# Performance work log

Measured on AMD Instinct MI355X. Metric: run time of the kernel, lower is better.

Reference implementation:

```python
import jax, jax.numpy as jnp
import numpy as np

N_NODES = 50000
N_EDGES = 500000
N_GRAPHS = 256
F_XD = 78


def _linear_init(key, fan_in, fan_out):
    s = 1.0 / np.sqrt(fan_in)
    kw, kb = jax.random.split(key)
    W = jax.random.uniform(kw, (fan_in, fan_out), jnp.float32, -s, s)
    b = jax.random.uniform(kb, (fan_out,), jnp.float32, -s, s)
    return W, b


def setup_inputs() -> dict:
    key = jax.random.key(0)
    ks = jax.random.split(key, 12)
    x = jax.random.normal(ks[0], (N_NODES, F_XD), jnp.float32)
    edge_index = jax.random.randint(ks[1], (2, N_EDGES), 0, N_NODES, jnp.int32)
    # sorted graph assignment; every graph non-empty
    batch = ((jnp.arange(N_NODES) * N_GRAPHS) // N_NODES).astype(jnp.int32)
    T = jax.random.normal(ks[2], (N_GRAPHS,), jnp.float32)
    P = jax.random.normal(ks[3], (N_GRAPHS,), jnp.float32)
    W1, b1 = _linear_init(ks[4], F_XD, F_XD)
    W2, b2 = _linear_init(ks[5], F_XD, 2 * F_XD)
    W3, b3 = _linear_init(ks[6], 2 * F_XD, 4 * F_XD)
    Wg1, bg1 = _linear_init(ks[7], 4 * F_XD, 1024)
    Wg2, bg2 = _linear_init(ks[8], 1024, 128)
    Wf1, bf1 = _linear_init(ks[9], 130, 1024)
    Wf2, bf2 = _linear_init(ks[10], 1024, 512)
    Wo, bo = _linear_init(ks[11], 512, 1)
    return dict(x=x, edge_index=edge_index, batch=batch, T=T, P=P,
                W1=W1, b1=b1, W2=W2, b2=b2, W3=W3, b3=b3,
                Wg1=Wg1, bg1=bg1, Wg2=Wg2, bg2=bg2,
                Wf1=Wf1, bf1=bf1, Wf2=Wf2, bf2=bf2, Wo=Wo, bo=bo)


def _gcn_conv(x, W, b, src, dst, norm, n_nodes):
    # PyG GCNConv: out = scatter_add(norm * (xW)[src] -> dst) + b
    h = x @ W
    msg = h[src] * norm[:, None]  # [E+N, F_out] gather, memory-bound
    return jax.ops.segment_sum(msg, dst, num_segments=n_nodes) + b


def reference(x, edge_index, batch, T, P,
              W1, b1, W2, b2, W3, b3,
              Wg1, bg1, Wg2, bg2, Wf1, bf1, Wf2, bf2, Wo, bo):
    n = x.shape[0]
    loops = jnp.arange(n, dtype=edge_index.dtype)
    src = jnp.concatenate([edge_index[0], loops])
    dst = jnp.concatenate([edge_index[1], loops])
    # symmetric normalization deg^-1/2 (A+I) deg^-1/2
    deg = jax.ops.segment_sum(jnp.ones_like(dst, dtype=x.dtype), dst, num_segments=n)
    dinv = jax.lax.rsqrt(deg)  # deg >= 1 due to self loops
    norm = dinv[src] * dinv[dst]

    h = jax.nn.relu(_gcn_conv(x, W1, b1, src, dst, norm, n))
    h = jax.nn.relu(_gcn_conv(h, W2, b2, src, dst, norm, n))
    h = jax.nn.relu(_gcn_conv(h, W3, b3, src, dst, norm, n))

    # global max pool per graph
    g = jax.ops.segment_max(h, batch, num_segments=N_GRAPHS)
    g = jax.nn.relu(g @ Wg1 + bg1)  # dropout = identity (eval)
    g = g @ Wg2 + bg2

    xc = jnp.concatenate([g, T[:, None], P[:, None]], axis=1)  # [G, 130]
    xc = jax.nn.relu(xc @ Wf1 + bf1)
    xc = jax.nn.relu(xc @ Wf2 + bf2)
    return xc @ Wo + bo
```

## Files before the change

kernel.cpp:

```cpp
#include <hip/hip_runtime.h>
#include <cstdint>
#include <cstddef>

static constexpr int NN = 50000;
static constexpr int NE = 500000;
static constexpr int NG = 256;

typedef short  frag8  __attribute__((ext_vector_type(8)));
typedef float  f32x4  __attribute__((ext_vector_type(4)));
typedef unsigned short us8 __attribute__((ext_vector_type(8)));

__device__ __forceinline__ unsigned short bf16_rne(float f) {
  unsigned u = __builtin_bit_cast(unsigned, f);
  u += 0x7fffu + ((u >> 16) & 1u);
  return (unsigned short)(u >> 16);
}
__device__ __forceinline__ float bf16_to_f(unsigned short h) {
  unsigned u = ((unsigned)h) << 16;
  return __builtin_bit_cast(float, u);
}

__global__ void k_count(const int* __restrict__ dst, int* __restrict__ cnt, int E) {
  int i = blockIdx.x * blockDim.x + threadIdx.x;
  if (i < E) atomicAdd(&cnt[dst[i]], 1);
}

__global__ void k_scan_partial(const int* __restrict__ cnt, int* __restrict__ partial,
                               float* __restrict__ dinv, int n) {
  __shared__ int sdata[1024];
  int tid = threadIdx.x;
  int i = blockIdx.x * 1024 + tid;
  int v = (i < n) ? cnt[i] : 0;
  if (i < n) dinv[i] = rsqrtf((float)(v + 1));
  sdata[tid] = v;
  __syncthreads();
  for (int s = 512; s > 0; s >>= 1) {
    if (tid < s) sdata[tid] += sdata[tid + s];
    __syncthreads();
  }
  if (tid == 0) partial[blockIdx.x] = sdata[0];
}

__global__ void k_scan_small(int* __restrict__ partial, int nb) {
  if (threadIdx.x == 0) {
    int run = 0;
    for (int b = 0; b < nb; ++b) { int v = partial[b]; partial[b] = run; run += v; }
  }
}

__global__ void k_scan_final(const int* __restrict__ cnt, const int* __restrict__ partial,
                             int* __restrict__ rowptr, int n) {
  __shared__ int buf[1024];
  int tid = threadIdx.x;
  int i = blockIdx.x * 1024 + tid;
  int v = (i < n) ? cnt[i] : 0;
  buf[tid] = v;
  __syncthreads();
  for (int off = 1; off < 1024; off <<= 1) {
    int t = (tid >= off) ? buf[tid - off] : 0;
    __syncthreads();
    buf[tid] += t;
    __syncthreads();
  }
  int excl = buf[tid] - v + partial[blockIdx.x];
  if (i < n) rowptr[i] = excl;
  if (i == n - 1) rowptr[n] = excl + v;
}

__global__ void k_fill(const int* __restrict__ src, const int* __restrict__ dst,
                       const int* __restrict__ rowptr, int* __restrict__ cur,
                       const float* __restrict__ dinv,
                       int* __restrict__ csr_src, float* __restrict__ csr_val, int E) {
  int i = blockIdx.x * blockDim.x + threadIdx.x;
  if (i < E) {
    int d = dst[i];
    int old = atomicAdd(&cur[d], -1);
    int pos = rowptr[d] + old - 1;
    int s = src[i];
    csr_src[pos] = s;
    csr_val[pos] = dinv[s];
  }
}

__global__ void k_padx(const float* __restrict__ x, float* __restrict__ x80) {
  int idx = blockIdx.x * blockDim.x + threadIdx.x;
  if (idx < NN * 80) {
    int row = idx / 80, c = idx - row * 80;
    x80[idx] = (c < 78) ? x[row * 78 + c] : 0.f;
  }
}

template<int CH, int CHP, int EPW>
__global__ void k_agg_dec8(const float* __restrict__ hin, const int* __restrict__ rowptr,
                           const int* __restrict__ csr_src, const float* __restrict__ csr_val,
                           const float* __restrict__ dinv,
                           unsigned short* __restrict__ Ah, unsigned short* __restrict__ Al, int n) {
  constexpr int Kp = CHP * 8;
  int wid = (blockIdx.x * blockDim.x + threadIdx.x) >> 6;
  int lane = threadIdx.x & 63;
  if (wid >= n) return;
  const float4* hin4 = (const float4*)hin;
  int eoff = lane / CH;
  int fl = lane - eoff * CH;
  float a[8];
#pragma unroll
  for (int j = 0; j < 8; ++j) a[j] = 0.f;
  int e0 = rowptr[wid], e1 = rowptr[wid + 1];
  if (eoff < EPW) {
    int e = e0 + eoff;
    for (; e + EPW < e1; e += 2 * EPW) {
      int   s0 = csr_src[e];        float w0 = csr_val[e];
      int   s1 = csr_src[e + EPW];  float w1 = csr_val[e + EPW];
      float4 u0 = hin4[(size_t)s0 * (CH * 2) + fl * 2];
      float4 u1 = hin4[(size_t)s0 * (CH * 2) + fl * 2 + 1];
      float4 v0 = hin4[(size_t)s1 * (CH * 2) + fl * 2];
      float4 v1 = hin4[(size_t)s1 * (CH * 2) + fl * 2 + 1];
      a[0] += w0 * u0.x + w1 * v0.x;  a[1] += w0 * u0.y + w1 * v0.y;
      a[2] += w0 * u0.z + w1 * v0.z;  a[3] += w0 * u0.w + w1 * v0.w;
      a[4] += w0 * u1.x + w1 * v1.x;  a[5] += w0 * u1.y + w1 * v1.y;
      a[6] += w0 * u1.z + w1 * v1.z;  a[7] += w0 * u1.w + w1 * v1.w;
    }
    if (e < e1) {
      int s0 = csr_src[e]; float w0 = csr_val[e];
      float4 u0 = hin4[(size_t)s0 * (CH * 2) + fl * 2];
      float4 u1 = hin4[(size_t)s0 * (CH * 2) + fl * 2 + 1];
      a[0] += w0 * u0.x; a[1] += w0 * u0.y; a[2] += w0 * u0.z; a[3] += w0 * u0.w;
      a[4] += w0 * u1.x; a[5] += w0 * u1.y; a[6] += w0 * u1.z; a[7] += w0 * u1.w;
    }
  }
  float r[8];
#pragma unroll
  for (int j = 0; j < 8; ++j) r[j] = a[j];
#pragma unroll
  for (int g = 1; g < EPW; ++g) {
#pragma unroll
    for (int j = 0; j < 8; ++j) r[j] += __shfl(a[j], lane + g * CH);
  }
  if (lane < CH) {
    float dv = dinv[wid];
    float4 s0 = hin4[(size_t)wid * (CH * 2) + lane * 2];
    float4 s1 = hin4[(size_t)wid * (CH * 2) + lane * 2 + 1];
    float v[8] = { dv * (r[0] + dv * s0.x), dv * (r[1] + dv * s0.y),
                   dv * (r[2] + dv * s0.z), dv * (r[3] + dv * s0.w),
                   dv * (r[4] + dv * s1.x), dv * (r[5] + dv * s1.y),
                   dv * (r[6] + dv * s1.z), dv * (r[7] + dv * s1.w) };
    us8 hi, lo;
#pragma unroll
    for (int j = 0; j < 8; ++j) {
      unsigned short h = bf16_rne(v[j]);
      hi[j] = h;
      lo[j] = bf16_rne(v[j] - bf16_to_f(h));
    }
    size_t base = (size_t)wid * Kp + lane * 8;
    *(us8*)(Ah + base) = hi;
    *(us8*)(Al + base) = lo;
  } else if (lane >= 60) {
    int c = CH + (lane - 60);
    if (c < CHP) {
      us8 z;
#pragma unroll
      for (int j = 0; j < 8; ++j) z[j] = 0;
      size_t base = (size_t)wid * Kp + (size_t)c * 8;
      *(us8*)(Ah + base) = z;
      *(us8*)(Al + base) = z;
    }
  }
}

template<int K, int N, int Kp, int Np>
__global__ void k_wdec(const float* __restrict__ W, unsigned short* __restrict__ Wh,
                       unsigned short* __restrict__ Wl) {
  int idx = blockIdx.x * blockDim.x + threadIdx.x;
  if (idx >= Np * Kp) return;
  int n = idx / Kp, k = idx - n * Kp;
  float v = (n < N && k < K) ? W[k * N + n] : 0.f;
  unsigned short h = bf16_rne(v);
  Wh[idx] = h;
  Wl[idx] = bf16_rne(v - bf16_to_f(h));
}

template<int Kp, int Np, int NB, bool POOL>
__global__ __launch_bounds__(256) void k_mm_mfma(const unsigned short* __restrict__ Ahp,
                                                 const unsigned short* __restrict__ Alp,
                                                 const unsigned short* __restrict__ Wh,
                                                 const unsigned short* __restrict__ Wl,
                                                 const float* __restrict__ bias,
                                                 float* __restrict__ C,
                                                 const int* __restrict__ batch,
                                                 unsigned int* __restrict__ poolU,
                                                 int N, int M) {
  constexpr int NCB = Np / NB;
  constexpr int NT = NB / 16;
  constexpr int KS = Kp / 32;
  constexpr int KC = Kp / 8;
  constexpr int PITCH = Kp + 8;
  __shared__ unsigned short wlds[2 * NB * PITCH];
  unsigned short* whi = wlds;
  unsigned short* wlo = wlds + NB * PITCH;
  int tid = threadIdx.x;
  int w = tid >> 6, l = tid & 63;
  int m = l & 15, kg = l >> 4;
  int nwg = gridDim.x;
  int orig = blockIdx.x;
  int qd = nwg >> 3, rm = nwg & 7;
  int xcd = orig & 7, seq = orig >> 3;
  int wgid = (xcd < rm ? xcd * (qd + 1) : rm * (qd + 1) + (xcd - rm) * qd) + seq;
  int bc = wgid % NCB;
  int br = wgid / NCB;
  int row0 = br * 128;
  for (int i = tid; i < 2 * NB * KC; i += 256) {
    int mtx = i / (NB * KC);
    int j = i - mtx * (NB * KC);
    int n = j / KC, qq = j - n * KC;
    const unsigned short* src = mtx ? Wl : Wh;
    unsigned short* dst = mtx ? wlo : whi;
    *(us8*)&dst[n * PITCH + qq * 8] = *(const us8*)&src[(size_t)(bc * NB + n) * Kp + qq * 8];
  }
  frag8 ah0[KS], al0[KS], ah1[KS], al1[KS];
  size_t arow0 = (size_t)(row0 + 32 * w + m) * Kp + kg * 8;
  size_t arow1 = arow0 + (size_t)16 * Kp;
#pragma unroll
  for (int kk = 0; kk < KS; ++kk) {
    ah0[kk] = *(const frag8*)(Ahp + arow0 + kk * 32);
    al0[kk] = *(const frag8*)(Alp + arow0 + kk * 32);
    ah1[kk] = *(const frag8*)(Ahp + arow1 + kk * 32);
    al1[kk] = *(const frag8*)(Alp + arow1 + kk * 32);
  }
  __syncthreads();

  f32x4 zero4 = {0.f, 0.f, 0.f, 0.f};
  f32x4 acc0[NT], acc1[NT];
#pragma unroll
  for (int t = 0; t < NT; ++t) { acc0[t] = zero4; acc1[t] = zero4; }

#pragma unroll
  for (int kk = 0; kk < KS; ++kk) {
#pragma unroll
    for (int t = 0; t < NT; ++t) {
      int n = t * 16 + m;
      int co = kk * 32 + kg * 8;
      frag8 bh = *(const frag8*)&whi[n * PITCH + co];
      frag8 bl = *(const frag8*)&wlo[n * PITCH + co];
      acc0[t] = __builtin_amdgcn_mfma_f32_16x16x32_bf16(ah0[kk], bh, acc0[t], 0, 0, 0);
      acc0[t] = __builtin_amdgcn_mfma_f32_16x16x32_bf16(ah0[kk], bl, acc0[t], 0, 0, 0);
      acc0[t] = __builtin_amdgcn_mfma_f32_16x16x32_bf16(al0[kk], bh, acc0[t], 0, 0, 0);
      acc1[t] = __builtin_amdgcn_mfma_f32_16x16x32_bf16(ah1[kk], bh, acc1[t], 0, 0, 0);
      acc1[t] = __builtin_amdgcn_mfma_f32_16x16x32_bf16(ah1[kk], bl, acc1[t], 0, 0, 0);
      acc1[t] = __builtin_amdgcn_mfma_f32_16x16x32_bf16(al1[kk], bh, acc1[t], 0, 0, 0);
    }
  }
  if (!POOL) {
#pragma unroll
    for (int t = 0; t < NT; ++t) {
      int col = bc * NB + t * 16 + m;
      float b = (col < N) ? bias[col] : 0.f;
#pragma unroll
      for (int r = 0; r < 4; ++r) {
        int row = row0 + 32 * w + kg * 4 + r;
        float v0 = fmaxf(acc0[t][r] + b, 0.f);
        float v1 = fmaxf(acc1[t][r] + b, 0.f);
        C[(size_t)row * Np + col] = (col < N) ? v0 : 0.f;
        C[(size_t)(row + 16) * Np + col] = (col < N) ? v1 : 0.f;
      }
    }
  } else {
    int gA = batch[row0];
    int rbase = row0 + 32 * w + kg * 4;
    int cls[8];
#pragma unroll
    for (int r = 0; r < 4; ++r) {
      int ra = rbase + r, rb = rbase + 16 + r;
      cls[r]     = (ra < M) ? ((batch[ra] == gA) ? 1 : 2) : 0;
      cls[4 + r] = (rb < M) ? ((batch[rb] == gA) ? 1 : 2) : 0;
    }
#pragma unroll
    for (int t = 0; t < NT; ++t) {
      int col = bc * NB + t * 16 + m;
      float b = (col < N) ? bias[col] : 0.f;
      float m0 = 0.f, m1 = 0.f;
#pragma unroll
      for (int r = 0; r < 4; ++r) {
        float v0 = fmaxf(acc0[t][r] + b, 0.f);
        float v1 = fmaxf(acc1[t][r] + b, 0.f);
        if (cls[r] == 1)     m0 = fmaxf(m0, v0); else if (cls[r] == 2)     m1 = fmaxf(m1, v0);
        if (cls[4 + r] == 1) m0 = fmaxf(m0, v1); else if (cls[4 + r] == 2) m1 = fmaxf(m1, v1);
      }
      m0 = fmaxf(m0, __shfl_xor(m0, 16)); m0 = fmaxf(m0, __shfl_xor(m0, 32));
      m1 = fmaxf(m1, __shfl_xor(m1, 16)); m1 = fmaxf(m1, __shfl_xor(m1, 32));
      if (l < 16 && col < N) {
        if (m0 > 0.f) atomicMax(&poolU[(size_t)gA * 320 + col], __float_as_uint(m0));
        if (m1 > 0.f) atomicMax(&poolU[(size_t)(gA + 1) * 320 + col], __float_as_uint(m1));
      }
    }
  }
}

template<int Kp, int Np, int NB, int KSPLIT, bool RELU, int OUTMODE, int SOUT>
__global__ __launch_bounds__(256) void k_hmm(const unsigned short* __restrict__ Ahp,
                                             const unsigned short* __restrict__ Alp,
                                             const unsigned short* __restrict__ Wh,
                                             const unsigned short* __restrict__ Wl,
                                             const float* __restrict__ bias,
                                             float* __restrict__ partOrC,
                                             unsigned short* __restrict__ OutH,
                                             unsigned short* __restrict__ OutL) {
  constexpr int NCB = Np / NB;
  constexpr int NT = NB / 16;
  constexpr int KS = Kp / 32 / KSPLIT;
  constexpr int PITCH = 40;
  __shared__ unsigned short wlds[2 * NB * PITCH];
  unsigned short* whi = wlds;
  unsigned short* wlo = wlds + NB * PITCH;
  int tid = threadIdx.x;
  int w = tid >> 6, l = tid & 63;
  int m = l & 15, kg = l >> 4;
  int bc = blockIdx.x % NCB;
  int kc = (blockIdx.x / NCB) % KSPLIT;
  int br = blockIdx.x / (NCB * KSPLIT);
  int row0 = br * 64;
  int kk0 = kc * KS;
  f32x4 zero4 = {0.f, 0.f, 0.f, 0.f};
  f32x4 acc[NT];
#pragma unroll
  for (int t = 0; t < NT; ++t) acc[t] = zero4;

  for (int kk = 0; kk < KS; ++kk) {
    int kabs = (kk0 + kk) * 32;
    for (int i = tid; i < NB * 8; i += 256) {
      int mtx = i / (NB * 4);
      int j = i - mtx * (NB * 4);
      int n = j >> 2, q = j & 3;
      const unsigned short* src = mtx ? Wl : Wh;
      unsigned short* dst = mtx ? wlo : whi;
      *(us8*)&dst[n * PITCH + ((q ^ (n >> 3)) & 3) * 8] =
          *(const us8*)&src[(size_t)(bc * NB + n) * Kp + kabs + q * 8];
    }
    __syncthreads();
    size_t abase = (size_t)(row0 + 16 * w + m) * Kp + kabs + kg * 8;
    frag8 ah = *(const frag8*)(Ahp + abase);
    frag8 al = *(const frag8*)(Alp + abase);
#pragma unroll
    for (int t = 0; t < NT; ++t) {
      int n = t * 16 + m;
      int sc = ((kg ^ (n >> 3)) & 3) * 8;
      frag8 bh = *(const frag8*)&whi[n * PITCH + sc];
      frag8 bl = *(const frag8*)&wlo[n * PITCH + sc];
      acc[t] = __builtin_amdgcn_mfma_f32_16x16x32_bf16(ah, bh, acc[t], 0, 0, 0);
      acc[t] = __builtin_amdgcn_mfma_f32_16x16x32_bf16(ah, bl, acc[t], 0, 0, 0);
      acc[t] = __builtin_amdgcn_mfma_f32_16x16x32_bf16(al, bh, acc[t], 0, 0, 0);
    }
    __syncthreads();
  }
#pragma unroll
  for (int t = 0; t < NT; ++t) {
    int col = bc * NB + t * 16 + m;
#pragma unroll
    for (int r = 0; r < 4; ++r) {
      int row = row0 + 16 * w + kg * 4 + r;
      float v = acc[t][r];
      if (KSPLIT > 1) {
        partOrC[((size_t)(kc * 256) + row) * Np + col] = v;
      } else {
        v += bias[col];
        if (RELU) v = fmaxf(v, 0.f);
        if (OUTMODE == 0) {
          partOrC[(size_t)row * SOUT + col] = v;
        } else {
          unsigned short h = bf16_rne(v);
          OutH[(size_t)row * SOUT + col] = h;
          OutL[(size_t)row * SOUT + col] = bf16_rne(v - bf16_to_f(h));
        }
      }
    }
  }
}

template<int Np, int KSPLIT, bool RELU, int OUTMODE, int SOUT>
__global__ void k_comb(const float* __restrict__ part, const float* __restrict__ bias,
                       float* __restrict__ Cf, unsigned short* __restrict__ OutH,
                       unsigned short* __restrict__ OutL) {
  int idx = blockIdx.x * 256 + threadIdx.x;
  int row = idx / Np, col = idx - row * Np;
  float s = bias[col];
#pragma unroll
  for (int kc = 0; kc < KSPLIT; ++kc) s += part[((size_t)(kc * 256) + row) * Np + col];
  if (RELU) s = fmaxf(s, 0.f);
  if (OUTMODE == 0) {
    Cf[(size_t)row * SOUT + col] = s;
  } else {
    unsigned short h = bf16_rne(s);
    OutH[(size_t)row * SOUT + col] = h;
    OutL[(size_t)row * SOUT + col] = bf16_rne(s - bf16_to_f(h));
  }
}

__global__ void k_pool_dec(const unsigned int* __restrict__ poolU,
                           unsigned short* __restrict__ g0H, unsigned short* __restrict__ g0L) {
  int idx = blockIdx.x * 256 + threadIdx.x;
  float v = __uint_as_float(poolU[idx]);
  unsigned short h = bf16_rne(v);
  g0H[idx] = h;
  g0L[idx] = bf16_rne(v - bf16_to_f(h));
}

__global__ void k_tp(const float* __restrict__ T, const float* __restrict__ P,
                     unsigned short* __restrict__ xcH, unsigned short* __restrict__ xcL) {
  int m = threadIdx.x;
  float t = T[m], p = P[m];
  unsigned short th = bf16_rne(t), ph = bf16_rne(p);
  xcH[(size_t)m * 160 + 128] = th;
  xcL[(size_t)m * 160 + 128] = bf16_rne(t - bf16_to_f(th));
  xcH[(size_t)m * 160 + 129] = ph;
  xcL[(size_t)m * 160 + 129] = bf16_rne(p - bf16_to_f(ph));
}

__global__ void k_final(const float* __restrict__ g4, const float* __restrict__ Wo,
                        const float* __restrict__ bo, float* __restrict__ out) {
  int g = blockIdx.x;
  int lane = threadIdx.x;
  float acc = 0.f;
#pragma unroll
  for (int u = 0; u < 8; ++u) {
    int k = lane + u * 64;
    acc += g4[(size_t)g * 512 + k] * Wo[k];
  }
  for (int s = 32; s > 0; s >>= 1) acc += __shfl_down(acc, s);
  if (lane == 0) out[g] = acc + bo[0];
}

extern "C" void kernel_launch(void* const* d_in, const int* in_sizes, int n_in,
                              void* d_out, int out_size, void* d_ws, size_t ws_size,
                              hipStream_t stream) {
  const float* x   = (const float*)d_in[0];
  const int*   ei  = (const int*)d_in[1];
  const int*   bat = (const int*)d_in[2];
  const float* T   = (const float*)d_in[3];
  const float* P   = (const float*)d_in[4];
  const float* W1  = (const float*)d_in[5];
  const float* b1  = (const float*)d_in[6];
  const float* W2  = (const float*)d_in[7];
  const float* b2  = (const float*)d_in[8];
  const float* W3  = (const float*)d_in[9];
  const float* b3  = (const float*)d_in[10];
  const float* Wg1 = (const float*)d_in[11];
  const float* bg1 = (const float*)d_in[12];
  const float* Wg2 = (const float*)d_in[13];
  const float* bg2 = (const float*)d_in[14];
  const float* Wf1 = (const float*)d_in[15];
  const float* bf1 = (const float*)d_in[16];
  const float* Wf2 = (const float*)d_in[17];
  const float* bf2 = (const float*)d_in[18];
  const float* Wo  = (const float*)d_in[19];
  const float* bo  = (const float*)d_in[20];
  float* out = (float*)d_out;

  char* ws = (char*)d_ws;
  size_t off = 0;
  auto alloc = [&](size_t bytes) -> void* {
    void* p = ws + off;
    off = (off + bytes + 255) & ~(size_t)255;
    return p;
  };
  float* Rbig    = (float*)alloc((size_t)(NN + 64) * 320 * 4);
  float* x80     = Rbig;
  float* h1      = Rbig;
  float* h2      = Rbig + (size_t)(NN + 64) * 80;
  unsigned short* aggH = (unsigned short*)alloc((size_t)(NN + 64) * 160 * 2);
  unsigned short* aggL = (unsigned short*)alloc((size_t)(NN + 64) * 160 * 2);
  unsigned short* wtH  = (unsigned short*)alloc((size_t)320 * 160 * 2);
  unsigned short* wtL  = (unsigned short*)alloc((size_t)320 * 160 * 2);
  int*   cnt     = (int*)alloc((size_t)NN * 4);
  int*   rowptr  = (int*)alloc((size_t)(NN + 1) * 4);
  int*   partial = (int*)alloc(64 * 4);
  int*   csr_src = (int*)alloc((size_t)NE * 4);
  float* csr_val = (float*)alloc((size_t)NE * 4);
  float* dinv    = (float*)alloc((size_t)NN * 4);
  unsigned short* wg1H = (unsigned short*)alloc((size_t)1024 * 320 * 2);
  unsigned short* wg1L = (unsigned short*)alloc((size_t)1024 * 320 * 2);
  unsigned short* wg2H = (unsigned short*)alloc((size_t)128 * 1024 * 2);
  unsigned short* wg2L = (unsigned short*)alloc((size_t)128 * 1024 * 2);
  unsigned short* wf1H = (unsigned short*)alloc((size_t)1024 * 160 * 2);
  unsigned short* wf1L = (unsigned short*)alloc((size_t)1024 * 160 * 2);
  unsigned short* wf2H = (unsigned short*)alloc((size_t)512 * 1024 * 2);
  unsigned short* wf2L = (unsigned short*)alloc((size_t)512 * 1024 * 2);
  unsigned int*  poolU = (unsigned int*)alloc((size_t)256 * 320 * 4);
  unsigned short* g0H = (unsigned short*)alloc((size_t)256 * 320 * 2);
  unsigned short* g0L = (unsigned short*)alloc((size_t)256 * 320 * 2);
  unsigned short* g1H = (unsigned short*)alloc((size_t)256 * 1024 * 2);
  unsigned short* g1L = (unsigned short*)alloc((size_t)256 * 1024 * 2);
  unsigned short* xcH = (unsigned short*)alloc((size_t)256 * 160 * 2);
  unsigned short* xcL = (unsigned short*)alloc((size_t)256 * 160 * 2);
  unsigned short* g3H = (unsigned short*)alloc((size_t)256 * 1024 * 2);
  unsigned short* g3L = (unsigned short*)alloc((size_t)256 * 1024 * 2);
  float* g4      = (float*)alloc((size_t)256 * 512 * 4);
  float* hpart   = (float*)alloc((size_t)8 * 256 * 512 * 4);
  (void)ws_size; (void)in_sizes; (void)n_in; (void)out_size;

  const int* srcp = ei;
  const int* dstp = ei + NE;

  hipMemsetAsync(cnt, 0, (size_t)NN * 4, stream);
  hipMemsetAsync(poolU, 0, (size_t)256 * 320 * 4, stream);
  hipMemsetAsync(xcH, 0, (size_t)256 * 160 * 2, stream);
  hipMemsetAsync(xcL, 0, (size_t)256 * 160 * 2, stream);

  k_count<<<(NE + 255) / 256, 256, 0, stream>>>(dstp, cnt, NE);
  int nb = (NN + 1023) / 1024;
  k_scan_partial<<<nb, 1024, 0, stream>>>(cnt, partial, dinv, NN);
  k_scan_small<<<1, 64, 0, stream>>>(partial, nb);
  k_scan_final<<<nb, 1024, 0, stream>>>(cnt, partial, rowptr, NN);
  k_fill<<<(NE + 255) / 256, 256, 0, stream>>>(srcp, dstp, rowptr, cnt, dinv, csr_src, csr_val, NE);

  k_wdec<312, 1024, 320, 1024><<<(1024 * 320 + 255) / 256, 256, 0, stream>>>(Wg1, wg1H, wg1L);
  k_wdec<1024, 128, 1024, 128><<<(128 * 1024 + 255) / 256, 256, 0, stream>>>(Wg2, wg2H, wg2L);
  k_wdec<130, 1024, 160, 1024><<<(1024 * 160 + 255) / 256, 256, 0, stream>>>(Wf1, wf1H, wf1L);
  k_wdec<1024, 512, 1024, 512><<<(512 * 1024 + 255) / 256, 256, 0, stream>>>(Wf2, wf2H, wf2L);

  const int aggBlocks = (NN * 64) / 256;
  const int mmRows128 = (NN + 127) / 128;

  k_padx<<<(NN * 80 + 255) / 256, 256, 0, stream>>>(x, x80);

  k_agg_dec8<10, 12, 6><<<aggBlocks, 256, 0, stream>>>(x80, rowptr, csr_src, csr_val, dinv, aggH, aggL, NN);
  k_wdec<78, 78, 96, 80><<<(96 * 80 + 255) / 256, 256, 0, stream>>>(W1, wtH, wtL);
  k_mm_mfma<96, 80, 80, false><<<mmRows128, 256, 0, stream>>>(
      aggH, aggL, wtH, wtL, b1, h1, nullptr, nullptr, 78, NN);
  k_agg_dec8<10, 12, 6><<<aggBlocks, 256, 0, stream>>>(h1, rowptr, csr_src, csr_val, dinv, aggH, aggL, NN);
  k_wdec<78, 156, 96, 160><<<(96 * 160 + 255) / 256, 256, 0, stream>>>(W2, wtH, wtL);
  k_mm_mfma<96, 160, 80, false><<<mmRows128 * 2, 256, 0, stream>>>(
      aggH, aggL, wtH, wtL, b2, h2, nullptr, nullptr, 156, NN);
  k_agg_dec8<20, 20, 3><<<aggBlocks, 256, 0, stream>>>(h2, rowptr, csr_src, csr_val, dinv, aggH, aggL, NN);
  k_wdec<156, 312, 160, 320><<<(160 * 320 + 255) / 256, 256, 0, stream>>>(W3, wtH, wtL);
  k_mm_mfma<160, 320, 80, true><<<mmRows128 * 4, 256, 0, stream>>>(
      aggH, aggL, wtH, wtL, b3, nullptr, bat, poolU, 312, NN);

  k_pool_dec<<<320, 256, 0, stream>>>(poolU, g0H, g0L);

  k_hmm<320, 1024, 128, 1, true, 1, 1024><<<4 * 8, 256, 0, stream>>>(
      g0H, g0L, wg1H, wg1L, bg1, nullptr, g1H, g1L);
  k_hmm<1024, 128, 64, 8, false, 0, 0><<<4 * 2 * 8, 256, 0, stream>>>(
      g1H, g1L, wg2H, wg2L, nullptr, hpart, nullptr, nullptr);
  k_comb<128, 8, false, 1, 160><<<128, 256, 0, stream>>>(hpart, bg2, nullptr, xcH, xcL);
  k_tp<<<1, 256, 0, stream>>>(T, P, xcH, xcL);
  k_hmm<160, 1024, 128, 1, true, 1, 1024><<<4 * 8, 256, 0, stream>>>(
      xcH, xcL, wf1H, wf1L, bf1, nullptr, g3H, g3L);
  k_hmm<1024, 512, 128, 4, false, 0, 0><<<4 * 4 * 4, 256, 0, stream>>>(
      g3H, g3L, wf2H, wf2L, nullptr, hpart, nullptr, nullptr);
  k_comb<512, 4, true, 0, 512><<<512, 256, 0, stream>>>(hpart, bf2, g4, nullptr, nullptr);
  k_final<<<NG, 64, 0, stream>>>(g4, Wo, bo, out);
}
```

Baseline: 344.3 us.

## Merge prep kernels, fuse pool decode into MLP GEMM, restage head GEMMs

Folds edge counting, input padding and all weight bf16 hi/lo decompositions into a single prep kernel, and replaces four memsets with one over a contiguous zeroed region. The head GEMM kernel now stages its whole K slice of weights into LDS once and keeps the A fragments in registers. It also reads the pooled fp32 max directly and splits it into hi/lo inline, and the T/P write is folded into the combine kernel. Narrower N blocks raise the block counts for the small 256-row MLP GEMMs. Together these cut launch count and per-k-step barriers, in exchange for more LDS per block and a larger split-K partial buffer.

```diff
diff --git a/kernel.cpp b/kernel.cpp
--- a/kernel.cpp
+++ b/kernel.cpp
@@ -9,6 +9,7 @@
 typedef short  frag8  __attribute__((ext_vector_type(8)));
 typedef float  f32x4  __attribute__((ext_vector_type(4)));
 typedef unsigned short us8 __attribute__((ext_vector_type(8)));
+typedef unsigned int   u32x8 __attribute__((ext_vector_type(8)));
 
 __device__ __forceinline__ unsigned short bf16_rne(float f) {
   unsigned u = __builtin_bit_cast(unsigned, f);
@@ -20,9 +21,65 @@
   return __builtin_bit_cast(float, u);
 }
 
-__global__ void k_count(const int* __restrict__ dst, int* __restrict__ cnt, int E) {
-  int i = blockIdx.x * blockDim.x + threadIdx.x;
-  if (i < E) atomicAdd(&cnt[dst[i]], 1);
+template<int K, int N, int Kp, int Np>
+__device__ __forceinline__ void wdec_elem(const float* __restrict__ W,
+                                          unsigned short* __restrict__ Wh,
+                                          unsigned short* __restrict__ Wl, int idx) {
+  if (idx >= Np * Kp) return;
+  int n = idx / Kp, k = idx - n * Kp;
+  float v = (n < N && k < K) ? W[k * N + n] : 0.f;
+  unsigned short h = bf16_rne(v);
+  Wh[idx] = h;
+  Wl[idx] = bf16_rne(v - bf16_to_f(h));
+}
+
+static constexpr int PB_COUNT = (NE + 255) / 256;
+static constexpr int PB_PADX  = (NN * 80) / 256;
+static constexpr int PB_W1 = (96 * 80) / 256;
+static constexpr int PB_W2 = (96 * 160) / 256;
+static constexpr int PB_W3 = (160 * 320) / 256;
+static constexpr int PB_G1 = (320 * 1024) / 256;
+static constexpr int PB_G2 = (1024 * 128) / 256;
+static constexpr int PB_F1 = (160 * 1024) / 256;
+static constexpr int PB_F2 = (1024 * 512) / 256;
+static constexpr int PREP_BLOCKS = PB_COUNT + PB_PADX + PB_W1 + PB_W2 + PB_W3 + PB_G1 + PB_G2 + PB_F1 + PB_F2;
+
+__global__ void k_prep(const int* __restrict__ dst, int* __restrict__ cnt,
+                       const float* __restrict__ x, float* __restrict__ x80,
+                       const float* __restrict__ W1, unsigned short* wt1H, unsigned short* wt1L,
+                       const float* __restrict__ W2, unsigned short* wt2H, unsigned short* wt2L,
+                       const float* __restrict__ W3, unsigned short* wt3H, unsigned short* wt3L,
+                       const float* __restrict__ Wg1, unsigned short* wg1H, unsigned short* wg1L,
+                       const float* __restrict__ Wg2, unsigned short* wg2H, unsigned short* wg2L,
+                       const float* __restrict__ Wf1, unsigned short* wf1H, unsigned short* wf1L,
+                       const float* __restrict__ Wf2, unsigned short* wf2H, unsigned short* wf2L) {
+  int b = blockIdx.x, tid = threadIdx.x;
+  if (b < PB_COUNT) {
+    int i = b * 256 + tid;
+    if (i < NE) atomicAdd(&cnt[dst[i]], 1);
+    return;
+  }
+  b -= PB_COUNT;
+  if (b < PB_PADX) {
+    int i = b * 256 + tid;
+    int r = i / 80, c = i - r * 80;
+    x80[i] = (c < 78) ? x[r * 78 + c] : 0.f;
+    return;
+  }
+  b -= PB_PADX;
+  if (b < PB_W1) { wdec_elem<78, 78, 96, 80>(W1, wt1H, wt1L, b * 256 + tid); return; }
+  b -= PB_W1;
+  if (b < PB_W2) { wdec_elem<78, 156, 96, 160>(W2, wt2H, wt2L, b * 256 + tid); return; }
+  b -= PB_W2;
+  if (b < PB_W3) { wdec_elem<156, 312, 160, 320>(W3, wt3H, wt3L, b * 256 + tid); return; }
+  b -= PB_W3;
+  if (b < PB_G1) { wdec_elem<312, 1024, 320, 1024>(Wg1, wg1H, wg1L, b * 256 + tid); return; }
+  b -= PB_G1;
+  if (b < PB_G2) { wdec_elem<1024, 128, 1024, 128>(Wg2, wg2H, wg2L, b * 256 + tid); return; }
+  b -= PB_G2;
+  if (b < PB_F1) { wdec_elem<130, 1024, 160, 1024>(Wf1, wf1H, wf1L, b * 256 + tid); return; }
+  b -= PB_F1;
+  wdec_elem<1024, 512, 1024, 512>(Wf2, wf2H, wf2L, b * 256 + tid);
 }
 
 __global__ void k_scan_partial(const int* __restrict__ cnt, int* __restrict__ partial,
@@ -79,14 +136,6 @@
     int s = src[i];
     csr_src[pos] = s;
     csr_val[pos] = dinv[s];
-  }
-}
-
-__global__ void k_padx(const float* __restrict__ x, float* __restrict__ x80) {
-  int idx = blockIdx.x * blockDim.x + threadIdx.x;
-  if (idx < NN * 80) {
-    int row = idx / 80, c = idx - row * 80;
-    x80[idx] = (c < 78) ? x[row * 78 + c] : 0.f;
   }
 }
 
@@ -165,18 +214,6 @@
       *(us8*)(Al + base) = z;
     }
   }
-}
-
-template<int K, int N, int Kp, int Np>
-__global__ void k_wdec(const float* __restrict__ W, unsigned short* __restrict__ Wh,
-                       unsigned short* __restrict__ Wl) {
-  int idx = blockIdx.x * blockDim.x + threadIdx.x;
-  if (idx >= Np * Kp) return;
-  int n = idx / Kp, k = idx - n * Kp;
-  float v = (n < N && k < K) ? W[k * N + n] : 0.f;
-  unsigned short h = bf16_rne(v);
-  Wh[idx] = h;
-  Wl[idx] = bf16_rne(v - bf16_to_f(h));
 }
 
 template<int Kp, int Np, int NB, bool POOL>
@@ -295,19 +332,22 @@
   }
 }
 
-template<int Kp, int Np, int NB, int KSPLIT, bool RELU, int OUTMODE, int SOUT>
-__global__ __launch_bounds__(256) void k_hmm(const unsigned short* __restrict__ Ahp,
-                                             const unsigned short* __restrict__ Alp,
-                                             const unsigned short* __restrict__ Wh,
-                                             const unsigned short* __restrict__ Wl,
-                                             const float* __restrict__ bias,
-                                             float* __restrict__ partOrC,
-                                             unsigned short* __restrict__ OutH,
-                                             unsigned short* __restrict__ OutL) {
+template<int Kp, int Np, int NB, int KSPLIT, bool RELU, int OUTMODE, int SOUT, bool AU32>
+__global__ __launch_bounds__(256) void k_hmm2(const unsigned short* __restrict__ Ahp,
+                                              const unsigned short* __restrict__ Alp,
+                                              const unsigned int* __restrict__ Au,
+                                              const unsigned short* __restrict__ Wh,
+                                              const unsigned short* __restrict__ Wl,
+                                              const float* __restrict__ bias,
+                                              float* __restrict__ partOrC,
+                                              unsigned short* __restrict__ OutH,
+                                              unsigned short* __restrict__ OutL) {
   constexpr int NCB = Np / NB;
   constexpr int NT = NB / 16;
   constexpr int KS = Kp / 32 / KSPLIT;
-  constexpr int PITCH = 40;
+  constexpr int KSL = KS * 32;
+  constexpr int CH8 = KSL / 8;
+  constexpr int PITCH = KSL + 8;
   __shared__ unsigned short wlds[2 * NB * PITCH];
   unsigned short* whi = wlds;
   unsigned short* wlo = wlds + NB * PITCH;
@@ -318,38 +358,56 @@
   int kc = (blockIdx.x / NCB) % KSPLIT;
   int br = blockIdx.x / (NCB * KSPLIT);
   int row0 = br * 64;
-  int kk0 = kc * KS;
-  f32x4 zero4 = {0.f, 0.f, 0.f, 0.f};
+  int k0 = kc * KSL;
+  for (int i = tid; i < 2 * NB * CH8; i += 256) {
+    int mtx = i / (NB * CH8);
+    int j = i - mtx * (NB * CH8);
+    int n = j / CH8, q = j - n * CH8;
+    const unsigned short* src = mtx ? Wl : Wh;
+    unsigned short* dst = mtx ? wlo : whi;
+    *(us8*)&dst[n * PITCH + q * 8] = *(const us8*)&src[(size_t)(bc * NB + n) * Kp + k0 + q * 8];
+  }
+  frag8 ah[KS], al[KS];
+  int arow = row0 + 16 * w + m;
+  if (AU32) {
+#pragma unroll
+    for (int kk = 0; kk < KS; ++kk) {
+      u32x8 uv = *(const u32x8*)(Au + (size_t)arow * Kp + k0 + kk * 32 + kg * 8);
+      frag8 h8, l8;
+#pragma unroll
+      for (int j = 0; j < 8; ++j) {
+        float v = __uint_as_float(uv[j]);
+        unsigned short hh = bf16_rne(v);
+        h8[j] = (short)hh;
+        l8[j] = (short)bf16_rne(v - bf16_to_f(hh));
+      }
+      ah[kk] = h8; al[kk] = l8;
+    }
+  } else {
+    size_t abase = (size_t)arow * Kp + k0 + kg * 8;
+#pragma unroll
+    for (int kk = 0; kk < KS; ++kk) {
+      ah[kk] = *(const frag8*)(Ahp + abase + kk * 32);
+      al[kk] = *(const frag8*)(Alp + abase + kk * 32);
+    }
+  }
+  __syncthreads();
+
   f32x4 acc[NT];
 #pragma unroll
-  for (int t = 0; t < NT; ++t) acc[t] = zero4;
-
+  for (int t = 0; t < NT; ++t) acc[t] = (f32x4){0.f, 0.f, 0.f, 0.f};
+#pragma unroll
   for (int kk = 0; kk < KS; ++kk) {
-    int kabs = (kk0 + kk) * 32;
-    for (int i = tid; i < NB * 8; i += 256) {
-      int mtx = i / (NB * 4);
-      int j = i - mtx * (NB * 4);
-      int n = j >> 2, q = j & 3;
-      const unsigned short* src = mtx ? Wl : Wh;
-      unsigned short* dst = mtx ? wlo : whi;
-      *(us8*)&dst[n * PITCH + ((q ^ (n >> 3)) & 3) * 8] =
-          *(const us8*)&src[(size_t)(bc * NB + n) * Kp + kabs + q * 8];
-    }
-    __syncthreads();
-    size_t abase = (size_t)(row0 + 16 * w + m) * Kp + kabs + kg * 8;
-    frag8 ah = *(const frag8*)(Ahp + abase);
-    frag8 al = *(const frag8*)(Alp + abase);
 #pragma unroll
     for (int t = 0; t < NT; ++t) {
       int n = t * 16 + m;
-      int sc = ((kg ^ (n >> 3)) & 3) * 8;
-      frag8 bh = *(const frag8*)&whi[n * PITCH + sc];
-      frag8 bl = *(const frag8*)&wlo[n * PITCH + sc];
-      acc[t] = __builtin_amdgcn_mfma_f32_16x16x32_bf16(ah, bh, acc[t], 0, 0, 0);
-      acc[t] = __builtin_amdgcn_mfma_f32_16x16x32_bf16(ah, bl, acc[t], 0, 0, 0);
-      acc[t] = __builtin_amdgcn_mfma_f32_16x16x32_bf16(al, bh, acc[t], 0, 0, 0);
-    }
-    __syncthreads();
+      int co = kk * 32 + kg * 8;
+      frag8 bh = *(const frag8*)&whi[n * PITCH + co];
+      frag8 bl = *(const frag8*)&wlo[n * PITCH + co];
+      acc[t] = __builtin_amdgcn_mfma_f32_16x16x32_bf16(ah[kk], bh, acc[t], 0, 0, 0);
+      acc[t] = __builtin_amdgcn_mfma_f32_16x16x32_bf16(ah[kk], bl, acc[t], 0, 0, 0);
+      acc[t] = __builtin_amdgcn_mfma_f32_16x16x32_bf16(al[kk], bh, acc[t], 0, 0, 0);
+    }
   }
 #pragma unroll
   for (int t = 0; t < NT; ++t) {
@@ -375,10 +433,11 @@
   }
 }
 
-template<int Np, int KSPLIT, bool RELU, int OUTMODE, int SOUT>
+template<int Np, int KSPLIT, bool RELU, int OUTMODE, int SOUT, bool TP>
 __global__ void k_comb(const float* __restrict__ part, const float* __restrict__ bias,
                        float* __restrict__ Cf, unsigned short* __restrict__ OutH,
-                       unsigned short* __restrict__ OutL) {
+                       unsigned short* __restrict__ OutL,
+                       const float* __restrict__ T, const float* __restrict__ P) {
   int idx = blockIdx.x * 256 + threadIdx.x;
   int row = idx / Np, col = idx - row * Np;
   float s = bias[col];
@@ -392,26 +451,15 @@
     OutH[(size_t)row * SOUT + col] = h;
     OutL[(size_t)row * SOUT + col] = bf16_rne(s - bf16_to_f(h));
   }
-}
-
-__global__ void k_pool_dec(const unsigned int* __restrict__ poolU,
-                           unsigned short* __restrict__ g0H, unsigned short* __restrict__ g0L) {
-  int idx = blockIdx.x * 256 + threadIdx.x;
-  float v = __uint_as_float(poolU[idx]);
-  unsigned short h = bf16_rne(v);
-  g0H[idx] = h;
-  g0L[idx] = bf16_rne(v - bf16_to_f(h));
-}
-
-__global__ void k_tp(const float* __restrict__ T, const float* __restrict__ P,
-                     unsigned short* __restrict__ xcH, unsigned short* __restrict__ xcL) {
-  int m = threadIdx.x;
-  float t = T[m], p = P[m];
-  unsigned short th = bf16_rne(t), ph = bf16_rne(p);
-  xcH[(size_t)m * 160 + 128] = th;
-  xcL[(size_t)m * 160 + 128] = bf16_rne(t - bf16_to_f(th));
-  xcH[(size_t)m * 160 + 129] = ph;
-  xcL[(size_t)m * 160 + 129] = bf16_rne(p - bf16_to_f(ph));
+  if (TP && idx < 256) {
+    int g = idx;
+    float tv = T[g], pv = P[g];
+    unsigned short th = bf16_rne(tv), ph = bf16_rne(pv);
+    OutH[(size_t)g * SOUT + 128] = th;
+    OutL[(size_t)g * SOUT + 128] = bf16_rne(tv - bf16_to_f(th));
+    OutH[(size_t)g * SOUT + 129] = ph;
+    OutL[(size_t)g * SOUT + 129] = bf16_rne(pv - bf16_to_f(ph));
+  }
 }
 
 __global__ void k_final(const float* __restrict__ g4, const float* __restrict__ Wo,
@@ -461,15 +509,24 @@
     off = (off + bytes + 255) & ~(size_t)255;
     return p;
   };
+  char* zero_base = ws + off;
+  int*           cnt   = (int*)alloc((size_t)NN * 4);
+  unsigned int*  poolU = (unsigned int*)alloc((size_t)256 * 320 * 4);
+  unsigned short* xcH  = (unsigned short*)alloc((size_t)256 * 160 * 2);
+  unsigned short* xcL  = (unsigned short*)alloc((size_t)256 * 160 * 2);
+  size_t zero_bytes = (size_t)((ws + off) - zero_base);
   float* Rbig    = (float*)alloc((size_t)(NN + 64) * 320 * 4);
   float* x80     = Rbig;
   float* h1      = Rbig;
   float* h2      = Rbig + (size_t)(NN + 64) * 80;
   unsigned short* aggH = (unsigned short*)alloc((size_t)(NN + 64) * 160 * 2);
   unsigned short* aggL = (unsigned short*)alloc((size_t)(NN + 64) * 160 * 2);
-  unsigned short* wtH  = (unsigned short*)alloc((size_t)320 * 160 * 2);
-  unsigned short* wtL  = (unsigned short*)alloc((size_t)320 * 160 * 2);
-  int*   cnt     = (int*)alloc((size_t)NN * 4);
+  unsigned short* wt1H = (unsigned short*)alloc((size_t)96 * 80 * 2);
+  unsigned short* wt1L = (unsigned short*)alloc((size_t)96 * 80 * 2);
+  unsigned short* wt2H = (unsigned short*)alloc((size_t)96 * 160 * 2);
+  unsigned short* wt2L = (unsigned short*)alloc((size_t)96 * 160 * 2);
+  unsigned short* wt3H = (unsigned short*)alloc((size_t)160 * 320 * 2);
+  unsigned short* wt3L = (unsigned short*)alloc((size_t)160 * 320 * 2);
   int*   rowptr  = (int*)alloc((size_t)(NN + 1) * 4);
   int*   partial = (int*)alloc(64 * 4);
   int*   csr_src = (int*)alloc((size_t)NE * 4);
@@ -483,13 +540,8 @@
   unsigned short* wf1L = (unsigned short*)alloc((size_t)1024 * 160 * 2);
   unsigned short* wf2H = (unsigned short*)alloc((size_t)512 * 1024 * 2);
   unsigned short* wf2L = (unsigned short*)alloc((size_t)512 * 1024 * 2);
-  unsigned int*  poolU = (unsigned int*)alloc((size_t)256 * 320 * 4);
-  unsigned short* g0H = (unsigned short*)alloc((size_t)256 * 320 * 2);
-  unsigned short* g0L = (unsigned short*)alloc((size_t)256 * 320 * 2);
   unsigned short* g1H = (unsigned short*)alloc((size_t)256 * 1024 * 2);
   unsigned short* g1L = (unsigned short*)alloc((size_t)256 * 1024 * 2);
-  unsigned short* xcH = (unsigned short*)alloc((size_t)256 * 160 * 2);
-  unsigned short* xcL = (unsigned short*)alloc((size_t)256 * 160 * 2);
   unsigned short* g3H = (unsigned short*)alloc((size_t)256 * 1024 * 2);
   unsigned short* g3L = (unsigned short*)alloc((size_t)256 * 1024 * 2);
   float* g4      = (float*)alloc((size_t)256 * 512 * 4);
@@ -499,53 +551,40 @@
   const int* srcp = ei;
   const int* dstp = ei + NE;
 
-  hipMemsetAsync(cnt, 0, (size_t)NN * 4, stream);
-  hipMemsetAsync(poolU, 0, (size_t)256 * 320 * 4, stream);
-  hipMemsetAsync(xcH, 0, (size_t)256 * 160 * 2, stream);
-  hipMemsetAsync(xcL, 0, (size_t)256 * 160 * 2, stream);
-
-  k_count<<<(NE + 255) / 256, 256, 0, stream>>>(dstp, cnt, NE);
+  hipMemsetAsync(zero_base, 0, zero_bytes, stream);
+
+  k_prep<<<PREP_BLOCKS, 256, 0, stream>>>(dstp, cnt, x, x80,
+                                          W1, wt1H, wt1L, W2, wt2H, wt2L, W3, wt3H, wt3L,
+                                          Wg1, wg1H, wg1L, Wg2, wg2H, wg2L,
+                                          Wf1, wf1H, wf1L, Wf2, wf2H, wf2L);
   int nb = (NN + 1023) / 1024;
   k_scan_partial<<<nb, 1024, 0, stream>>>(cnt, partial, dinv, NN);
   k_scan_small<<<1, 64, 0, stream>>>(partial, nb);
   k_scan_final<<<nb, 1024, 0, stream>>>(cnt, partial, rowptr, NN);
   k_fill<<<(NE + 255) / 256, 256, 0, stream>>>(srcp, dstp, rowptr, cnt, dinv, csr_src, csr_val, NE);
 
-  k_wdec<312, 1024, 320, 1024><<<(1024 * 320 + 255) / 256, 256, 0, stream>>>(Wg1, wg1H, wg1L);
-  k_wdec<1024, 128, 1024, 128><<<(128 * 1024 + 255) / 256, 256, 0, stream>>>(Wg2, wg2H, wg2L);
-  k_wdec<130, 1024, 160, 1024><<<(1024 * 160 + 255) / 256, 256, 0, stream>>>(Wf1, wf1H, wf1L);
-  k_wdec<1024, 512, 1024, 512><<<(512 * 1024 + 255) / 256, 256, 0, stream>>>(Wf2, wf2H, wf2L);
-
   const int aggBlocks = (NN * 64) / 256;
   const int mmRows128 = (NN + 127) / 128;
 
-  k_padx<<<(NN * 80 + 255) / 256, 256, 0, stream>>>(x, x80);
-
   k_agg_dec8<10, 12, 6><<<aggBlocks, 256, 0, stream>>>(x80, rowptr, csr_src, csr_val, dinv, aggH, aggL, NN);
-  k_wdec<78, 78, 96, 80><<<(96 * 80 + 255) / 256, 256, 0, stream>>>(W1, wtH, wtL);
   k_mm_mfma<96, 80, 80, false><<<mmRows128, 256, 0, stream>>>(
-      aggH, aggL, wtH, wtL, b1, h1, nullptr, nullptr, 78, NN);
+      aggH, aggL, wt1H, wt1L, b1, h1, nullptr, nullptr, 78, NN);
   k_agg_dec8<10, 12, 6><<<aggBlocks, 256, 0, stream>>>(h1, rowptr, csr_src, csr_val, dinv, aggH, aggL, NN);
-  k_wdec<78, 156, 96, 160><<<(96 * 160 + 255) / 256, 256, 0, stream>>>(W2, wtH, wtL);
   k_mm_mfma<96, 160, 80, false><<<mmRows128 * 2, 256, 0, stream>>>(
-      aggH, aggL, wtH, wtL, b2, h2, nullptr, nullptr, 156, NN);
+      aggH, aggL, wt2H, wt2L, b2, h2, nullptr, nullptr, 156, NN);
   k_agg_dec8<20, 20, 3><<<aggBlocks, 256, 0, stream>>>(h2, rowptr, csr_src, csr_val, dinv, aggH, aggL, NN);
-  k_wdec<156, 312, 160, 320><<<(160 * 320 + 255) / 256, 256, 0, stream>>>(W3, wtH, wtL);
   k_mm_mfma<160, 320, 80, true><<<mmRows128 * 4, 256, 0, stream>>>(
-      aggH, aggL, wtH, wtL, b3, nullptr, bat, poolU, 312, NN);
-
-  k_pool_dec<<<320, 256, 0, stream>>>(poolU, g0H, g0L);
-
-  k_hmm<320, 1024, 128, 1, true, 1, 1024><<<4 * 8, 256, 0, stream>>>(
-      g0H, g0L, wg1H, wg1L, bg1, nullptr, g1H, g1L);
-  k_hmm<1024, 128, 64, 8, false, 0, 0><<<4 * 2 * 8, 256, 0, stream>>>(
-      g1H, g1L, wg2H, wg2L, nullptr, hpart, nullptr, nullptr);
-  k_comb<128, 8, false, 1, 160><<<128, 256, 0, stream>>>(hpart, bg2, nullptr, xcH, xcL);
-  k_tp<<<1, 256, 0, stream>>>(T, P, xcH, xcL);
-  k_hmm<160, 1024, 128, 1, true, 1, 1024><<<4 * 8, 256, 0, stream>>>(
-      xcH, xcL, wf1H, wf1L, bf1, nullptr, g3H, g3L);
-  k_hmm<1024, 512, 128, 4, false, 0, 0><<<4 * 4 * 4, 256, 0, stream>>>(
-      g3H, g3L, wf2H, wf2L, nullptr, hpart, nullptr, nullptr);
-  k_comb<512, 4, true, 0, 512><<<512, 256, 0, stream>>>(hpart, bf2, g4, nullptr, nullptr);
+      aggH, aggL, wt3H, wt3L, b3, nullptr, bat, poolU, 312, NN);
+
+  k_hmm2<320, 1024, 32, 1, true, 1, 1024, true><<<4 * 32, 256, 0, stream>>>(
+      nullptr, nullptr, poolU, wg1H, wg1L, bg1, nullptr, g1H, g1L);
+  k_hmm2<1024, 128, 32, 8, false, 0, 0, false><<<4 * 4 * 8, 256, 0, stream>>>(
+      g1H, g1L, nullptr, wg2H, wg2L, nullptr, hpart, nullptr, nullptr);
+  k_comb<128, 8, false, 1, 160, true><<<128, 256, 0, stream>>>(hpart, bg2, nullptr, xcH, xcL, T, P);
+  k_hmm2<160, 1024, 32, 1, true, 1, 1024, false><<<4 * 32, 256, 0, stream>>>(
+      xcH, xcL, nullptr, wf1H, wf1L, bf1, nullptr, g3H, g3L);
+  k_hmm2<1024, 512, 32, 8, false, 0, 0, false><<<4 * 16 * 8, 256, 0, stream>>>(
+      g3H, g3L, nullptr, wf2H, wf2L, nullptr, hpart, nullptr, nullptr);
+  k_comb<512, 8, true, 0, 512, false><<<512, 256, 0, stream>>>(hpart, bf2, g4, nullptr, nullptr, nullptr, nullptr);
   k_final<<<NG, 64, 0, stream>>>(g4, Wo, bo, out);
 }
```

Measured after the change: 286.7 us. -16.7%, faster.
